# Optimization experiments

Measured on AMD Instinct MI355X. Metric: run time of the kernel, lower is better.

Reference implementation:

```python
import jax, jax.numpy as jnp
import numpy as np

B, C, H, W = 4, 256, 64, 64

def _conv1x1(x, Wt, b):
    # x: [b,c,h,w], Wt: [out,in], b: [out]
    return jnp.einsum('bchw,dc->bdhw', x, Wt) + b[None, :, None, None]

def setup_inputs() -> dict:
    key = jax.random.key(0)
    ks = jax.random.split(key, 10)
    s = 1.0 / np.sqrt(C)
    return {
        'F_c': jax.random.normal(ks[0], (B, C, H, W), jnp.float32),
        'F_s': jax.random.normal(ks[1], (B, C, H, W), jnp.float32),
        'Wf': jax.random.normal(ks[2], (C, C), jnp.float32) * s,
        'bf': jnp.zeros((C,), jnp.float32),
        'Wg': jax.random.normal(ks[3], (C, C), jnp.float32) * s,
        'bg': jnp.zeros((C,), jnp.float32),
        'Wh': jax.random.normal(ks[4], (C, C), jnp.float32) * s,
        'bh': jnp.zeros((C,), jnp.float32),
        'Wo': jax.random.normal(ks[5], (C, C), jnp.float32) * s,
        'bo': jnp.zeros((C,), jnp.float32),
    }

def reference(F_c, F_s, Wf, bf, Wg, bg, Wh, bh, Wo, bo):
    b, c, h, w = F_c.shape
    Fq = _conv1x1(F_c, Wf, bf).reshape(b, c, -1)          # [b,c,Nc]
    G = _conv1x1(F_s, Wg, bg).reshape(b, c, -1)           # [b,c,Ns]
    Hv = _conv1x1(F_s, Wh, bh).reshape(b, c, -1)          # [b,c,Ns]
    S = jnp.einsum('bcn,bcm->bnm', Fq, G)                 # [b,Nc,Ns] (unscaled)
    S = jax.nn.softmax(S, axis=-1)
    res = jnp.einsum('bcm,bnm->bcn', Hv, S)               # [b,c,Nc]
    res = res.reshape(b, c, h, w)
    return _conv1x1(res, Wo, bo)
```

## Files before the change

### kernel.cpp

```cpp
#include <hip/hip_runtime.h>
#include <stdint.h>

#define NB 4
#define CC 256
#define NN 4096
#define KITERS 32
#define WAIT_LGKM0 0xC07F

typedef __attribute__((ext_vector_type(8))) _Float16 half8;
typedef __attribute__((ext_vector_type(4))) _Float16 half4;
typedef __attribute__((ext_vector_type(2))) _Float16 half2v;
typedef __attribute__((ext_vector_type(4))) float floatx4;
typedef __attribute__((ext_vector_type(16))) float float16v;
typedef __attribute__((ext_vector_type(4))) int intx4;

__device__ __forceinline__ void cvt16v(float4 a, float4 b, float4 c, float4 d,
                                       half8& lo, half8& hi) {
  lo[0] = (_Float16)a.x; lo[1] = (_Float16)a.y; lo[2] = (_Float16)a.z; lo[3] = (_Float16)a.w;
  lo[4] = (_Float16)b.x; lo[5] = (_Float16)b.y; lo[6] = (_Float16)b.z; lo[7] = (_Float16)b.w;
  hi[0] = (_Float16)c.x; hi[1] = (_Float16)c.y; hi[2] = (_Float16)c.z; hi[3] = (_Float16)c.w;
  hi[4] = (_Float16)d.x; hi[5] = (_Float16)d.y; hi[6] = (_Float16)d.z; hi[7] = (_Float16)d.w;
}

__global__ __launch_bounds__(256, 3) void k_qkv(const float* __restrict__ Fc,
                                                const float* __restrict__ Fs,
                                                const float* __restrict__ Wf,
                                                const float* __restrict__ Wg,
                                                const float* __restrict__ Wh,
                                                const float* __restrict__ bf,
                                                const float* __restrict__ bg,
                                                const float* __restrict__ bh,
                                                _Float16* __restrict__ Qs,
                                                _Float16* __restrict__ Ks,
                                                _Float16* __restrict__ Vs) {
  __shared__ float tmp[32][132];
  __shared__ _Float16 As[128][40];
  __shared__ _Float16 Bs[128][40];
  const int z = blockIdx.z, bz = blockIdx.y;
  const float* F = ((z == 0) ? Fc : Fs) + (size_t)bz * CC * NN;
  const float* W = (z == 0) ? Wf : ((z == 1) ? Wg : Wh);
  const float* bias = (z == 0) ? bf : ((z == 1) ? bg : bh);
  int mt, nt;
  if (z < 2) { mt = blockIdx.x >> 5; nt = blockIdx.x & 31; }
  else       { mt = blockIdx.x >> 1; nt = blockIdx.x & 1;  }
  const int m0 = mt * 128, n0 = nt * 128;
  const int xn0 = (z < 2) ? n0 : m0;
  const int wd0 = (z < 2) ? m0 : n0;
  const int tid = threadIdx.x;
  const int wave = tid >> 6, lane = tid & 63, quad = lane >> 4, l15 = lane & 15;
  const int wm = (wave >> 1) * 64, wn = (wave & 1) * 64;

  floatx4 acc[4][4];
#pragma unroll
  for (int i = 0; i < 4; i++)
#pragma unroll
    for (int j = 0; j < 4; j++) acc[i][j] = (floatx4){0.f, 0.f, 0.f, 0.f};

  const int srow = tid >> 1, shalf = (tid & 1) * 16;
  const int fc = tid >> 3, fn = (tid & 7) * 16;
  const int xr = tid >> 1, xh = (tid & 1) * 16;

  float4 wr0, wr1, wr2, wr3, fr0, fr1, fr2, fr3;
  {
    const float4* wp = (const float4*)(W + (size_t)(wd0 + srow) * 256 + 0 + shalf);
    wr0 = wp[0]; wr1 = wp[1]; wr2 = wp[2]; wr3 = wp[3];
    const float4* fp = (const float4*)(F + (size_t)(0 + fc) * NN + xn0 + fn);
    fr0 = fp[0]; fr1 = fp[1]; fr2 = fp[2]; fr3 = fp[3];
  }

  for (int kk = 0; kk < 256; kk += 32) {
    __syncthreads();
    *(float4*)&tmp[fc][fn + 0] = fr0;
    *(float4*)&tmp[fc][fn + 4] = fr1;
    *(float4*)&tmp[fc][fn + 8] = fr2;
    *(float4*)&tmp[fc][fn + 12] = fr3;
    half8 w_lo, w_hi;
    cvt16v(wr0, wr1, wr2, wr3, w_lo, w_hi);
    if (z < 2) {
      *(half8*)&As[srow][shalf] = w_lo;
      *(half8*)&As[srow][shalf + 8] = w_hi;
    } else {
      *(half8*)&Bs[srow][shalf] = w_lo;
      *(half8*)&Bs[srow][shalf + 8] = w_hi;
    }
    __syncthreads();
    if (kk + 32 < 256) {
      const float4* wp = (const float4*)(W + (size_t)(wd0 + srow) * 256 + kk + 32 + shalf);
      wr0 = wp[0]; wr1 = wp[1]; wr2 = wp[2]; wr3 = wp[3];
      const float4* fp = (const float4*)(F + (size_t)(kk + 32 + fc) * NN + xn0 + fn);
      fr0 = fp[0]; fr1 = fp[1]; fr2 = fp[2]; fr3 = fp[3];
    }
    half8 xlo, xhi;
#pragma unroll
    for (int i = 0; i < 8; i++) xlo[i] = (_Float16)tmp[xh + i][xr];
#pragma unroll
    for (int i = 0; i < 8; i++) xhi[i] = (_Float16)tmp[xh + 8 + i][xr];
    if (z < 2) {
      *(half8*)&Bs[xr][xh] = xlo;
      *(half8*)&Bs[xr][xh + 8] = xhi;
    } else {
      *(half8*)&As[xr][xh] = xlo;
      *(half8*)&As[xr][xh + 8] = xhi;
    }
    __syncthreads();
    half8 af[4], bfr[4];
#pragma unroll
    for (int mb = 0; mb < 4; mb++) af[mb] = *(const half8*)&As[wm + mb * 16 + l15][quad * 8];
#pragma unroll
    for (int nb = 0; nb < 4; nb++) bfr[nb] = *(const half8*)&Bs[wn + nb * 16 + l15][quad * 8];
#pragma unroll
    for (int mb = 0; mb < 4; mb++)
#pragma unroll
      for (int nb = 0; nb < 4; nb++)
        acc[mb][nb] = __builtin_amdgcn_mfma_f32_16x16x32_f16(af[mb], bfr[nb], acc[mb][nb], 0, 0, 0);
  }

  if (z < 2) {
    _Float16* op = (z == 0 ? Qs : Ks) + (size_t)bz * NN * CC;
#pragma unroll
    for (int mb = 0; mb < 4; mb++) {
      int d0 = m0 + wm + mb * 16 + quad * 4;
      float b0 = bias[d0], b1 = bias[d0 + 1], b2 = bias[d0 + 2], b3 = bias[d0 + 3];
      const int cs = d0 >> 4, hh = (d0 >> 3) & 1, j0 = d0 & 7;
#pragma unroll
      for (int nb = 0; nb < 4; nb++) {
        int n_ = n0 + wn + nb * 16 + l15;
        int kt = n_ >> 5, ql_ = n_ & 31;
        half4 pk;
        pk[0] = (_Float16)(acc[mb][nb][0] + b0);
        pk[1] = (_Float16)(acc[mb][nb][1] + b1);
        pk[2] = (_Float16)(acc[mb][nb][2] + b2);
        pk[3] = (_Float16)(acc[mb][nb][3] + b3);
        size_t idx = ((size_t)(kt * 16 + cs) * 64 + ql_ + 32 * hh) * 8 + j0;
        *(half4*)(op + idx) = pk;
      }
    }
  } else {
    _Float16* op = Vs + (size_t)bz * NN * CC;
#pragma unroll
    for (int mb = 0; mb < 4; mb++) {
      int nq0 = m0 + wm + mb * 16 + quad * 4;
      const int kt = nq0 >> 5, krel = nq0 & 31;
      const int hk = krel >> 4, hh = (krel >> 3) & 1, j0 = krel & 7;
#pragma unroll
      for (int nb = 0; nb < 4; nb++) {
        int d = n0 + wn + nb * 16 + l15;
        int ql_ = d & 31, g = (d >> 5) & 7;
        float bv = bias[d];
        half4 pk;
        pk[0] = (_Float16)(acc[mb][nb][0] + bv);
        pk[1] = (_Float16)(acc[mb][nb][1] + bv);
        pk[2] = (_Float16)(acc[mb][nb][2] + bv);
        pk[3] = (_Float16)(acc[mb][nb][3] + bv);
        size_t idx = (((size_t)(kt * 8 + g) * 2 + hk) * 64 + ql_ + 32 * hh) * 8 + j0;
        *(half4*)(op + idx) = pk;
      }
    }
  }
}

__global__ __launch_bounds__(256, 2) void k_attn(const _Float16* __restrict__ Q,
                                                 const _Float16* __restrict__ K,
                                                 const _Float16* __restrict__ Vt,
                                                 _Float16* __restrict__ Opart,
                                                 float2* __restrict__ Ml) {
  __shared__ _Float16 smem[8192 * 3 + 4096];
  const int tid = threadIdx.x;
  const int wave = tid >> 6, lane = tid & 63;
  _Float16* Kl = smem;
  _Float16* Plw = smem + 3 * 8192 + wave * 1024;

  const int qt = blockIdx.x, ck = blockIdx.y, b = blockIdx.z;
  const int ql = lane & 31, h = lane >> 5;
  const int q0 = qt * 128 + wave * 32;
  const _Float16* Qb = Q + (size_t)b * NN * CC;
  const _Float16* Kb = K + (size_t)b * NN * CC;
  const _Float16* Vb = Vt + (size_t)b * NN * CC;
  const int kt_base = ck * (1024 / 32);

  const int ktq = q0 >> 5;
  half8 qf[16];
#pragma unroll
  for (int cs = 0; cs < 16; cs++)
    qf[cs] = *(const half8*)(Qb + ((size_t)(ktq * 16 + cs) * 64 + lane) * 8);

  float16v Oa[8];
#pragma unroll
  for (int g = 0; g < 8; g++)
#pragma unroll
    for (int i = 0; i < 16; i++) Oa[g][i] = 0.f;

  float m_run = -1e30f, l_run = 0.f;

  intx4 kpre[4], vpre[4];
  {
    const _Float16* Kt = Kb + (size_t)kt_base * 8192;
    const _Float16* Vtile = Vb + (size_t)kt_base * 8192;
#pragma unroll
    for (int p = 0; p < 4; p++) {
      kpre[p] = *(const intx4*)(Kt + tid * 8 + p * 2048);
      vpre[p] = *(const intx4*)(Vtile + tid * 8 + p * 2048);
    }
  }

  for (int t = 0; t < KITERS; t++) {
    const int vb = t & 1;
    _Float16* Vw = smem + (1 + vb) * 8192;
    __syncthreads();
#pragma unroll
    for (int p = 0; p < 4; p++) {
      *(intx4*)(Kl + tid * 8 + p * 2048) = kpre[p];
      *(intx4*)(Vw + tid * 8 + p * 2048) = vpre[p];
    }
    __syncthreads();
    if (t + 1 < KITERS) {
      const _Float16* Kt = Kb + (size_t)(kt_base + t + 1) * 8192;
      const _Float16* Vtile = Vb + (size_t)(kt_base + t + 1) * 8192;
#pragma unroll
      for (int p = 0; p < 4; p++) {
        kpre[p] = *(const intx4*)(Kt + tid * 8 + p * 2048);
        vpre[p] = *(const intx4*)(Vtile + tid * 8 + p * 2048);
      }
    }

    float16v s, s2;
#pragma unroll
    for (int i = 0; i < 16; i++) { s[i] = 0.f; s2[i] = 0.f; }
    if (t > 0) {
      _Float16* Vr = smem + (1 + (vb ^ 1)) * 8192;
      half8 pf0 = *(const half8*)(Plw + lane * 8);
      half8 pf1 = *(const half8*)(Plw + 512 + lane * 8);
#pragma unroll
      for (int i = 0; i < 16; i++) {
        half8 kf = *(const half8*)(Kl + i * 512 + lane * 8);
        if (i & 1)
          s2 = __builtin_amdgcn_mfma_f32_32x32x16_f16(kf, qf[i], s2, 0, 0, 0);
        else
          s = __builtin_amdgcn_mfma_f32_32x32x16_f16(kf, qf[i], s, 0, 0, 0);
        const int u = i & 7, ks = i >> 3;
        half8 vf = *(const half8*)(Vr + (2 * u + ks) * 512 + lane * 8);
        Oa[u] = __builtin_amdgcn_mfma_f32_32x32x16_f16(vf, ks ? pf1 : pf0, Oa[u], 0, 0, 0);
      }
    } else {
#pragma unroll
      for (int cs = 0; cs < 16; cs += 2) {
        half8 kfa = *(const half8*)(Kl + cs * 512 + lane * 8);
        s = __builtin_amdgcn_mfma_f32_32x32x16_f16(kfa, qf[cs], s, 0, 0, 0);
        half8 kfb = *(const half8*)(Kl + (cs + 1) * 512 + lane * 8);
        s2 = __builtin_amdgcn_mfma_f32_32x32x16_f16(kfb, qf[cs + 1], s2, 0, 0, 0);
      }
    }
#pragma unroll
    for (int i = 0; i < 16; i++) s[i] += s2[i];

    float t0 = fmaxf(s[0], s[1]), t1 = fmaxf(s[2], s[3]);
    float t2 = fmaxf(s[4], s[5]), t3 = fmaxf(s[6], s[7]);
    float t4 = fmaxf(s[8], s[9]), t5 = fmaxf(s[10], s[11]);
    float t6 = fmaxf(s[12], s[13]), t7 = fmaxf(s[14], s[15]);
    t0 = fmaxf(t0, t1); t2 = fmaxf(t2, t3); t4 = fmaxf(t4, t5); t6 = fmaxf(t6, t7);
    float tmax = fmaxf(fmaxf(t0, t2), fmaxf(t4, t6));
    tmax = fmaxf(tmax, __shfl_xor(tmax, 32));
    bool need = tmax > m_run + 8.0f;
    if (__any((int)need)) {
      float mN = need ? tmax : m_run;
      float alpha = __expf(m_run - mN);
      m_run = mN;
      l_run *= alpha;
#pragma unroll
      for (int g = 0; g < 8; g++)
#pragma unroll
        for (int i = 0; i < 16; i++) Oa[g][i] *= alpha;
    }
#pragma unroll
    for (int i = 0; i < 16; i++) s[i] = __expf(s[i] - m_run);
    float u0 = (s[0] + s[1]) + (s[2] + s[3]);
    float u1 = (s[4] + s[5]) + (s[6] + s[7]);
    float u2 = (s[8] + s[9]) + (s[10] + s[11]);
    float u3 = (s[12] + s[13]) + (s[14] + s[15]);
    float ts = (u0 + u1) + (u2 + u3);
    ts += __shfl_xor(ts, 32);
    l_run += ts;
#pragma unroll
    for (int r = 0; r < 16; r += 2) {
      half2v pk;
      pk[0] = (_Float16)s[r];
      pk[1] = (_Float16)s[r + 1];
      int k = (r & 3) + 8 * (r >> 2) + 4 * h;
      *(half2v*)(Plw + (k >> 4) * 512 + (ql + 32 * ((k >> 3) & 1)) * 8 + (k & 7)) = pk;
    }
  }

  {
    _Float16* Vr = smem + (1 + ((KITERS - 1) & 1)) * 8192;
    half8 pf0 = *(const half8*)(Plw + lane * 8);
    half8 pf1 = *(const half8*)(Plw + 512 + lane * 8);
#pragma unroll
    for (int u = 0; u < 8; u++) {
      half8 vfa = *(const half8*)(Vr + (2 * u) * 512 + lane * 8);
      Oa[u] = __builtin_amdgcn_mfma_f32_32x32x16_f16(vfa, pf0, Oa[u], 0, 0, 0);
    }
#pragma unroll
    for (int u = 0; u < 8; u++) {
      half8 vfb = *(const half8*)(Vr + (2 * u + 1) * 512 + lane * 8);
      Oa[u] = __builtin_amdgcn_mfma_f32_32x32x16_f16(vfb, pf1, Oa[u], 0, 0, 0);
    }
  }

  float invl = 1.f / l_run;
  __syncthreads();
  float* ot = (float*)smem + wave * (32 * 33);
  _Float16* Opb = Opart + ((size_t)ck * NB + b) * NN * CC;
  const int qr = lane >> 1;
  const int chalf = (lane & 1) * 16;
#pragma unroll
  for (int g = 0; g < 8; g++) {
#pragma unroll
    for (int r = 0; r < 16; r++)
      ot[((r & 3) + 8 * (r >> 2) + 4 * h) * 33 + ql] = Oa[g][r] * invl;
    __builtin_amdgcn_s_waitcnt(WAIT_LGKM0);
    half8 o0, o1;
#pragma unroll
    for (int i = 0; i < 8; i++) o0[i] = (_Float16)ot[(chalf + i) * 33 + qr];
#pragma unroll
    for (int i = 0; i < 8; i++) o1[i] = (_Float16)ot[(chalf + 8 + i) * 33 + qr];
    _Float16* gp = Opb + (size_t)(q0 + qr) * CC + g * 32 + chalf;
    *(half8*)gp = o0;
    *(half8*)(gp + 8) = o1;
    __builtin_amdgcn_s_waitcnt(WAIT_LGKM0);
  }
  if (h == 0) {
    float2 ml; ml.x = m_run; ml.y = l_run;
    Ml[((size_t)ck * NB + b) * NN + q0 + ql] = ml;
  }
}

__global__ __launch_bounds__(256, 2) void k_out(const _Float16* __restrict__ Opart,
                                                const float2* __restrict__ Ml,
                                                const float* __restrict__ Wo,
                                                const float* __restrict__ bo,
                                                float* __restrict__ out) {
  __shared__ _Float16 As[64][40];
  __shared__ _Float16 Bs[128][40];
  const int bz = blockIdx.y;
  const int mt = blockIdx.x >> 1, nt = blockIdx.x & 1;
  const int m0 = mt * 64, n0 = nt * 128;
  const int tid = threadIdx.x;
  const int wave = tid >> 6, lane = tid & 63, quad = lane >> 4, l15 = lane & 15;
  const int wn = wave * 32;

  floatx4 acc[4][2];
#pragma unroll
  for (int i = 0; i < 4; i++)
#pragma unroll
    for (int j = 0; j < 2; j++) acc[i][j] = (floatx4){0.f, 0.f, 0.f, 0.f};

  const int arow = tid >> 2, acol = (tid & 3) * 8;
  const int brow = tid >> 1, bcol = (tid & 1) * 16;

  const size_t qi = (size_t)bz * NN + m0 + arow;
  float2 a0 = Ml[qi], a1 = Ml[(size_t)NB * NN + qi];
  float2 a2 = Ml[(size_t)2 * NB * NN + qi], a3 = Ml[(size_t)3 * NB * NN + qi];
  float M = fmaxf(fmaxf(a0.x, a1.x), fmaxf(a2.x, a3.x));
  float w0 = __expf(a0.x - M) * a0.y, w1 = __expf(a1.x - M) * a1.y;
  float w2 = __expf(a2.x - M) * a2.y, w3 = __expf(a3.x - M) * a3.y;
  float inv = 1.f / (w0 + w1 + w2 + w3);
  w0 *= inv; w1 *= inv; w2 *= inv; w3 *= inv;
  const size_t ps = (size_t)NB * NN * CC;
  const _Float16* prow = Opart + qi * CC;

  half8 pA0, pA1, pA2, pA3;
  float4 wr0, wr1, wr2, wr3;
  {
    const _Float16* pr = prow + acol;
    pA0 = *(const half8*)pr;
    pA1 = *(const half8*)(pr + ps);
    pA2 = *(const half8*)(pr + 2 * ps);
    pA3 = *(const half8*)(pr + 3 * ps);
    const float4* wp = (const float4*)(Wo + (size_t)(n0 + brow) * 256 + bcol);
    wr0 = wp[0]; wr1 = wp[1]; wr2 = wp[2]; wr3 = wp[3];
  }

  for (int kk = 0; kk < 256; kk += 32) {
    half8 ma;
#pragma unroll
    for (int i = 0; i < 8; i++)
      ma[i] = (_Float16)(w0 * (float)pA0[i] + w1 * (float)pA1[i] +
                         w2 * (float)pA2[i] + w3 * (float)pA3[i]);
    half8 b_lo, b_hi;
    cvt16v(wr0, wr1, wr2, wr3, b_lo, b_hi);
    __syncthreads();
    *(half8*)&As[arow][acol] = ma;
    *(half8*)&Bs[brow][bcol] = b_lo;
    *(half8*)&Bs[brow][bcol + 8] = b_hi;
    __syncthreads();
    if (kk + 32 < 256) {
      const _Float16* pr = prow + kk + 32 + acol;
      pA0 = *(const half8*)pr;
      pA1 = *(const half8*)(pr + ps);
      pA2 = *(const half8*)(pr + 2 * ps);
      pA3 = *(const half8*)(pr + 3 * ps);
      const float4* wp = (const float4*)(Wo + (size_t)(n0 + brow) * 256 + kk + 32 + bcol);
      wr0 = wp[0]; wr1 = wp[1]; wr2 = wp[2]; wr3 = wp[3];
    }
    half8 af[4], bfr[2];
#pragma unroll
    for (int mb = 0; mb < 4; mb++) af[mb] = *(const half8*)&As[mb * 16 + l15][quad * 8];
#pragma unroll
    for (int nb = 0; nb < 2; nb++) bfr[nb] = *(const half8*)&Bs[wn + nb * 16 + l15][quad * 8];
#pragma unroll
    for (int mb = 0; mb < 4; mb++)
#pragma unroll
      for (int nb = 0; nb < 2; nb++)
        acc[mb][nb] = __builtin_amdgcn_mfma_f32_16x16x32_f16(af[mb], bfr[nb], acc[mb][nb], 0, 0, 0);
  }

  float* op = out + (size_t)bz * NN * CC;
#pragma unroll
  for (int mb = 0; mb < 4; mb++) {
    int nq0 = m0 + mb * 16 + quad * 4;
#pragma unroll
    for (int nb = 0; nb < 2; nb++) {
      int d = n0 + wn + nb * 16 + l15;
      float bv = bo[d];
      floatx4 pk;
      pk[0] = acc[mb][nb][0] + bv;
      pk[1] = acc[mb][nb][1] + bv;
      pk[2] = acc[mb][nb][2] + bv;
      pk[3] = acc[mb][nb][3] + bv;
      *(floatx4*)(op + (size_t)d * NN + nq0) = pk;
    }
  }
}

extern "C" void kernel_launch(void* const* d_in, const int* in_sizes, int n_in,
                              void* d_out, int out_size, void* d_ws, size_t ws_size,
                              hipStream_t stream) {
  const float* Fc = (const float*)d_in[0];
  const float* Fs = (const float*)d_in[1];
  const float* Wf = (const float*)d_in[2];
  const float* bf_ = (const float*)d_in[3];
  const float* Wg = (const float*)d_in[4];
  const float* bg = (const float*)d_in[5];
  const float* Wh = (const float*)d_in[6];
  const float* bh = (const float*)d_in[7];
  const float* Wo = (const float*)d_in[8];
  const float* bo = (const float*)d_in[9];

  char* ws = (char*)d_ws;
  const size_t sz = (size_t)NB * NN * CC * sizeof(_Float16);
  _Float16* Opart = (_Float16*)(ws + 0 * sz);
  _Float16* Qs = (_Float16*)(ws + 4 * sz);
  _Float16* Ks = (_Float16*)(ws + 5 * sz);
  _Float16* Vs = (_Float16*)(ws + 6 * sz);
  float2* Ml = (float2*)(ws + 7 * sz);

  k_qkv<<<dim3(64, NB, 3), 256, 0, stream>>>(Fc, Fs, Wf, Wg, Wh, bf_, bg, bh, Qs, Ks, Vs);
  k_attn<<<dim3(32, 4, NB), 256, 0, stream>>>(Qs, Ks, Vs, Opart, Ml);
  k_out<<<dim3(128, NB), 256, 0, stream>>>(Opart, Ml, Wo, bo, (float*)d_out);
}
```

Measured before the change: 213.4 us.

## Stream K/V tiles via global_load_lds and keep P in registers with permlane swap

The attention loop now loads K and V tiles straight into LDS with global_load_lds, which removes the register staging and the LDS stores, and double-buffers K so each iteration needs one barrier instead of two. The softmax probabilities are packed to fp16 and rearranged across lanes with permlane32_swap into MFMA B-operand registers, replacing the LDS round trip through a per-wave P buffer. MFMA sections also run at raised wave priority. This trades more LDS (four 8K-half buffers) and an explicit vmcnt wait for less VGPR pressure and fewer LDS operations.

```diff
diff --git a/kernel.cpp b/kernel.cpp
--- a/kernel.cpp
+++ b/kernel.cpp
@@ -20,6 +20,17 @@
   lo[4] = (_Float16)b.x; lo[5] = (_Float16)b.y; lo[6] = (_Float16)b.z; lo[7] = (_Float16)b.w;
   hi[0] = (_Float16)c.x; hi[1] = (_Float16)c.y; hi[2] = (_Float16)c.z; hi[3] = (_Float16)c.w;
   hi[4] = (_Float16)d.x; hi[5] = (_Float16)d.y; hi[6] = (_Float16)d.z; hi[7] = (_Float16)d.w;
+}
+
+__device__ __forceinline__ int packh2(float a, float b) {
+  half2v p; p[0] = (_Float16)a; p[1] = (_Float16)b;
+  return __builtin_bit_cast(int, p);
+}
+
+__device__ __forceinline__ void a16(const _Float16* g, _Float16* l) {
+  __builtin_amdgcn_global_load_lds(
+      (__attribute__((address_space(1))) void*)(uintptr_t)g,
+      (__attribute__((address_space(3))) void*)l, 16, 0, 0);
 }
 
 __global__ __launch_bounds__(256, 3) void k_qkv(const float* __restrict__ Fc,
@@ -164,19 +175,19 @@
                                                  const _Float16* __restrict__ Vt,
                                                  _Float16* __restrict__ Opart,
                                                  float2* __restrict__ Ml) {
-  __shared__ _Float16 smem[8192 * 3 + 4096];
+  __shared__ _Float16 smem[8192 * 4];
   const int tid = threadIdx.x;
   const int wave = tid >> 6, lane = tid & 63;
-  _Float16* Kl = smem;
-  _Float16* Plw = smem + 3 * 8192 + wave * 1024;
 
   const int qt = blockIdx.x, ck = blockIdx.y, b = blockIdx.z;
   const int ql = lane & 31, h = lane >> 5;
   const int q0 = qt * 128 + wave * 32;
   const _Float16* Qb = Q + (size_t)b * NN * CC;
-  const _Float16* Kb = K + (size_t)b * NN * CC;
-  const _Float16* Vb = Vt + (size_t)b * NN * CC;
-  const int kt_base = ck * (1024 / 32);
+  const _Float16* Kg = K + (size_t)b * NN * CC;
+  const _Float16* Vg = Vt + (size_t)b * NN * CC;
+  const int kt_base = ck * KITERS;
+  const int so = wave * 512;
+  const int go = wave * 512 + lane * 8;
 
   const int ktq = q0 >> 5;
   half8 qf[16];
@@ -191,45 +202,39 @@
     for (int i = 0; i < 16; i++) Oa[g][i] = 0.f;
 
   float m_run = -1e30f, l_run = 0.f;
-
-  intx4 kpre[4], vpre[4];
+  half8 pf0, pf1;
+#pragma unroll
+  for (int i = 0; i < 8; i++) { pf0[i] = (_Float16)0.f; pf1[i] = (_Float16)0.f; }
+
   {
-    const _Float16* Kt = Kb + (size_t)kt_base * 8192;
-    const _Float16* Vtile = Vb + (size_t)kt_base * 8192;
-#pragma unroll
-    for (int p = 0; p < 4; p++) {
-      kpre[p] = *(const intx4*)(Kt + tid * 8 + p * 2048);
-      vpre[p] = *(const intx4*)(Vtile + tid * 8 + p * 2048);
-    }
+    const _Float16* Kt = Kg + (size_t)kt_base * 8192;
+#pragma unroll
+    for (int p = 0; p < 4; p++) a16(Kt + p * 2048 + go, smem + p * 2048 + so);
   }
 
   for (int t = 0; t < KITERS; t++) {
-    const int vb = t & 1;
-    _Float16* Vw = smem + (1 + vb) * 8192;
-    __syncthreads();
-#pragma unroll
-    for (int p = 0; p < 4; p++) {
-      *(intx4*)(Kl + tid * 8 + p * 2048) = kpre[p];
-      *(intx4*)(Vw + tid * 8 + p * 2048) = vpre[p];
-    }
-    __syncthreads();
-    if (t + 1 < KITERS) {
-      const _Float16* Kt = Kb + (size_t)(kt_base + t + 1) * 8192;
-      const _Float16* Vtile = Vb + (size_t)(kt_base + t + 1) * 8192;
-#pragma unroll
-      for (int p = 0; p < 4; p++) {
-        kpre[p] = *(const intx4*)(Kt + tid * 8 + p * 2048);
-        vpre[p] = *(const intx4*)(Vtile + tid * 8 + p * 2048);
+    asm volatile("s_waitcnt vmcnt(0)" ::: "memory");
+    __builtin_amdgcn_s_barrier();
+    {
+      const _Float16* Vtile = Vg + (size_t)(kt_base + t) * 8192;
+      _Float16* Vw = smem + (2 + (t & 1)) * 8192;
+#pragma unroll
+      for (int p = 0; p < 4; p++) a16(Vtile + p * 2048 + go, Vw + p * 2048 + so);
+      if (t + 1 < KITERS) {
+        const _Float16* Kt = Kg + (size_t)(kt_base + t + 1) * 8192;
+        _Float16* Kw = smem + ((t + 1) & 1) * 8192;
+#pragma unroll
+        for (int p = 0; p < 4; p++) a16(Kt + p * 2048 + go, Kw + p * 2048 + so);
       }
     }
+    const _Float16* Kl = smem + (t & 1) * 8192;
 
     float16v s, s2;
 #pragma unroll
     for (int i = 0; i < 16; i++) { s[i] = 0.f; s2[i] = 0.f; }
+    __builtin_amdgcn_s_setprio(1);
     if (t > 0) {
-      _Float16* Vr = smem + (1 + (vb ^ 1)) * 8192;
-      half8 pf0 = *(const half8*)(Plw + lane * 8);
-      half8 pf1 = *(const half8*)(Plw + 512 + lane * 8);
+      const _Float16* Vr = smem + (2 + ((t - 1) & 1)) * 8192;
 #pragma unroll
       for (int i = 0; i < 16; i++) {
         half8 kf = *(const half8*)(Kl + i * 512 + lane * 8);
@@ -250,6 +255,7 @@
         s2 = __builtin_amdgcn_mfma_f32_32x32x16_f16(kfb, qf[cs + 1], s2, 0, 0, 0);
       }
     }
+    __builtin_amdgcn_s_setprio(0);
 #pragma unroll
     for (int i = 0; i < 16; i++) s[i] += s2[i];
 
@@ -280,20 +286,28 @@
     float ts = (u0 + u1) + (u2 + u3);
     ts += __shfl_xor(ts, 32);
     l_run += ts;
-#pragma unroll
-    for (int r = 0; r < 16; r += 2) {
-      half2v pk;
-      pk[0] = (_Float16)s[r];
-      pk[1] = (_Float16)s[r + 1];
-      int k = (r & 3) + 8 * (r >> 2) + 4 * h;
-      *(half2v*)(Plw + (k >> 4) * 512 + (ql + 32 * ((k >> 3) & 1)) * 8 + (k & 7)) = pk;
-    }
-  }
-
+
+    {
+      int A01 = packh2(s[0], s[1]), B23 = packh2(s[2], s[3]);
+      int C45 = packh2(s[4], s[5]), D67 = packh2(s[6], s[7]);
+      int E01 = packh2(s[8], s[9]), F23 = packh2(s[10], s[11]);
+      int G45 = packh2(s[12], s[13]), H67 = packh2(s[14], s[15]);
+      auto rA = __builtin_amdgcn_permlane32_swap(A01, C45, false, false);
+      auto rB = __builtin_amdgcn_permlane32_swap(B23, D67, false, false);
+      auto rC = __builtin_amdgcn_permlane32_swap(E01, G45, false, false);
+      auto rD = __builtin_amdgcn_permlane32_swap(F23, H67, false, false);
+      intx4 w0, w1;
+      w0[0] = rA[0]; w0[1] = rB[0]; w0[2] = rA[1]; w0[3] = rB[1];
+      w1[0] = rC[0]; w1[1] = rD[0]; w1[2] = rC[1]; w1[3] = rD[1];
+      pf0 = __builtin_bit_cast(half8, w0);
+      pf1 = __builtin_bit_cast(half8, w1);
+    }
+  }
+
+  asm volatile("s_waitcnt vmcnt(0)" ::: "memory");
+  __builtin_amdgcn_s_barrier();
   {
-    _Float16* Vr = smem + (1 + ((KITERS - 1) & 1)) * 8192;
-    half8 pf0 = *(const half8*)(Plw + lane * 8);
-    half8 pf1 = *(const half8*)(Plw + 512 + lane * 8);
+    const _Float16* Vr = smem + (2 + ((KITERS - 1) & 1)) * 8192;
 #pragma unroll
     for (int u = 0; u < 8; u++) {
       half8 vfa = *(const half8*)(Vr + (2 * u) * 512 + lane * 8);
```

Result: faster. 200.8 us (-5.9%).
